# Kernel tuning notes

Measured on AMD Instinct MI355X. Metric: run time of the kernel, lower is better.

The kernel has to match this reference:

```python
import jax, jax.numpy as jnp
import numpy as np

K = 4
G = 64
IN_DIM = 256
OUT_DIM = 256
BATCH = 512
T0, T1 = -1.0, 1.0


def setup_inputs() -> dict:
    key = jax.random.key(0)
    kx, kw = jax.random.split(key)
    x = jax.random.uniform(kx, (BATCH, IN_DIM), jnp.float32, T0, T1)
    # xavier_normal_ on [G+K, in, out]: std = sqrt(2 / (fan_in + fan_out)) with fan over last two dims
    std = (2.0 / (IN_DIM + OUT_DIM)) ** 0.5
    w = jax.random.normal(kw, (G + K, IN_DIM, OUT_DIM), jnp.float32) * std
    # knot vector: k-1 repeats of t0, linspace(t0,t1,G+1), k-1 repeats of t1
    t = jnp.concatenate([
        jnp.full((K - 1,), T0, jnp.float32),
        jnp.linspace(T0, T1, G + 1, dtype=jnp.float32),
        jnp.full((K - 1,), T1, jnp.float32),
    ])
    return {"x": x, "w": w, "t": t, "k": K}


def _basis(x, t, k):
    """Cox-de Boor: the k nonzero order-k B-spline basis values at each x.
    Returns (idx, N): idx [..., k] basis indices i-k+1..i, N [..., k] values."""
    n_t = t.shape[0]
    # interval i with t[i] <= x < t[i+1], clipped to the valid span
    i = jnp.clip(jnp.searchsorted(t, x, side='right') - 1, k - 1, n_t - k - 1)
    N = jnp.ones(x.shape + (1,), x.dtype)
    for p in range(1, k):  # static small loop (k=4)
        jj = jnp.arange(1, p + 1)
        left = x[..., None] - t[i[..., None] + 1 - jj]   # [..., p]
        right = t[i[..., None] + jj] - x[..., None]      # [..., p]
        saved = jnp.zeros_like(x)
        vals = []
        for r in range(p):
            d = right[..., r] + left[..., p - 1 - r]      # t[i+r+1] - t[i+r+1-p]
            temp = N[..., r] / d
            vals.append(saved + right[..., r] * temp)
            saved = left[..., p - 1 - r] * temp
        vals.append(saved)
        N = jnp.stack(vals, -1)
    idx = i[..., None] - (k - 1) + jnp.arange(k)
    return idx, N


def reference(x, w, t, k):
    in_dim = x.shape[1]
    n_rows = w.shape[0]
    idx, y1 = _basis(x, t, k)                             # [B,in,k], [B,in,k]
    # last row of w (index -1 == n_rows-1) weights the SiLU residual term
    idx_full = jnp.concatenate(
        [idx, jnp.full(idx.shape[:-1] + (1,), n_rows - 1, idx.dtype)], -1)  # [B,in,k+1]
    silu = x * jax.nn.sigmoid(x)
    y2 = jnp.concatenate([y1, silu[..., None]], -1)       # [B,in,k+1]
    # gather local spline coefficients: w2[b,c,j,o] = w[idx_full[b,c,j], c, o]
    w2 = w[idx_full, jnp.arange(in_dim)[None, :, None], :]  # [B,in,k+1,out]
    return jnp.einsum('bcjo,bcj->bo', w2, y2)             # [B,out]
```

## Files before the change

### kernel.cpp

```cpp
#include <hip/hip_runtime.h>
#include <math.h>

#define IN_DIM  256
#define OUT_DIM 256
#define NROWS   68
#define NT      71
#define BATCH   512

__global__ __launch_bounds__(256) void kan_gather_kernel(
    const float* __restrict__ x, const float* __restrict__ w,
    const float* __restrict__ t, float* __restrict__ out) {
  __shared__ float  lt[NT];
  __shared__ float4 lyv[64];
  __shared__ float  lys[64];
  __shared__ int    lbase[64];
  __shared__ float4 red4[4][64];

  const int tid = threadIdx.x;
  const unsigned bid = blockIdx.x;
  const int sl = (bid & 7) >> 1;
  const int b  = ((bid & 1) << 8) | (bid >> 3);

  if (tid < NT) lt[tid] = t[tid];
  __syncthreads();

  if (tid < 64) {
    const int c = sl * 64 + tid;
    const float xv = x[b * IN_DIM + c];
    int i = 3 + (int)floorf((xv + 1.0f) * 32.0f);
    i = i < 3 ? 3 : (i > 66 ? 66 : i);
    while (i > 3 && xv < lt[i]) --i;
    while (i < 66 && xv >= lt[i + 1]) ++i;

    float N0 = 1.f, N1 = 0.f, N2 = 0.f, N3 = 0.f;
    {
      const float l1 = xv - lt[i];
      const float r1 = lt[i + 1] - xv;
      const float tp = N0 / (r1 + l1);
      N1 = l1 * tp;
      N0 = r1 * tp;
    }
    {
      const float l1 = xv - lt[i];
      const float l2 = xv - lt[i - 1];
      const float r1 = lt[i + 1] - xv;
      const float r2 = lt[i + 2] - xv;
      float saved = 0.f;
      const float tp0 = N0 / (r1 + l2);
      const float n0 = saved + r1 * tp0; saved = l2 * tp0;
      const float tp1 = N1 / (r2 + l1);
      const float n1 = saved + r2 * tp1; saved = l1 * tp1;
      N0 = n0; N1 = n1; N2 = saved;
    }
    {
      const float l1 = xv - lt[i];
      const float l2 = xv - lt[i - 1];
      const float l3 = xv - lt[i - 2];
      const float r1 = lt[i + 1] - xv;
      const float r2 = lt[i + 2] - xv;
      const float r3 = lt[i + 3] - xv;
      float saved = 0.f;
      const float tp0 = N0 / (r1 + l3);
      const float n0 = saved + r1 * tp0; saved = l3 * tp0;
      const float tp1 = N1 / (r2 + l2);
      const float n1 = saved + r2 * tp1; saved = l2 * tp1;
      const float tp2 = N2 / (r3 + l1);
      const float n2 = saved + r3 * tp2; saved = l1 * tp2;
      N0 = n0; N1 = n1; N2 = n2; N3 = saved;
    }
    lyv[tid]   = make_float4(N0, N1, N2, N3);
    lys[tid]   = xv / (1.0f + expf(-xv));
    lbase[tid] = i - 3;
  }
  __syncthreads();

  const int oq = tid & 63;
  const int cs = tid >> 6;
  const float4* __restrict__ w4 = (const float4*)w;

  float4 acc = make_float4(0.f, 0.f, 0.f, 0.f);
  const int cbeg = cs * 16;
  #pragma unroll 2
  for (int m = 0; m < 16; ++m) {
    const int cl = cbeg + m;
    const float4 yv = lyv[cl];
    const float  ys = lys[cl];
    const int base  = lbase[cl];
    const float4* p = w4 + (sl * 64 + cl) * 64 + oq;
    const float4 a0 = p[(base + 0) * 16384];
    const float4 a1 = p[(base + 1) * 16384];
    const float4 a2 = p[(base + 2) * 16384];
    const float4 a3 = p[(base + 3) * 16384];
    const float4 a4 = p[67 * 16384];
    acc.x += yv.x * a0.x + yv.y * a1.x + yv.z * a2.x + yv.w * a3.x + ys * a4.x;
    acc.y += yv.x * a0.y + yv.y * a1.y + yv.z * a2.y + yv.w * a3.y + ys * a4.y;
    acc.z += yv.x * a0.z + yv.y * a1.z + yv.z * a2.z + yv.w * a3.z + ys * a4.z;
    acc.w += yv.x * a0.w + yv.y * a1.w + yv.z * a2.w + yv.w * a3.w + ys * a4.w;
  }

  red4[cs][oq] = acc;
  __syncthreads();
  if (tid < 64) {
    const float4 p0 = red4[0][oq];
    const float4 p1 = red4[1][oq];
    const float4 p2 = red4[2][oq];
    const float4 p3 = red4[3][oq];
    float* op = out + b * OUT_DIM + oq * 4;
    atomicAdd(op + 0, (p0.x + p1.x) + (p2.x + p3.x));
    atomicAdd(op + 1, (p0.y + p1.y) + (p2.y + p3.y));
    atomicAdd(op + 2, (p0.z + p1.z) + (p2.z + p3.z));
    atomicAdd(op + 3, (p0.w + p1.w) + (p2.w + p3.w));
  }
}

extern "C" void kernel_launch(void* const* d_in, const int* in_sizes, int n_in,
                              void* d_out, int out_size, void* d_ws, size_t ws_size,
                              hipStream_t stream) {
  const float* x = (const float*)d_in[0];
  const float* w = (const float*)d_in[1];
  const float* t = (const float*)d_in[2];
  float* out = (float*)d_out;
  hipMemsetAsync(out, 0, (size_t)out_size * sizeof(float), stream);
  kan_gather_kernel<<<BATCH * 4, 256, 0, stream>>>(x, w, t, out);
}
```

Measured before the change: 95.41 us.

## Convert weights to bf16 in a pre-pass and gather half-width rows

Adds a conversion kernel that rounds the full fp32 weight tensor to bf16 in workspace on every call. The gather kernel then reads bf16 weights as uint4 (8 outputs per thread), so each gathered row carries half the bytes, and the cross-thread reduction is reorganised into 8 channel slices over 32 output lanes. The conversion pass itself reads all weights and writes half, which is about as much traffic as the gather saves. It also lowers the weight precision.

```diff
diff --git a/kernel.cpp b/kernel.cpp
--- a/kernel.cpp
+++ b/kernel.cpp
@@ -1,20 +1,51 @@
 #include <hip/hip_runtime.h>
 #include <math.h>
+#include <stdint.h>
 
 #define IN_DIM  256
 #define OUT_DIM 256
 #define NROWS   68
 #define NT      71
 #define BATCH   512
+#define W_ELEMS (NROWS * IN_DIM * OUT_DIM)
+
+__device__ __forceinline__ uint32_t bf16_rne(float f) {
+  uint32_t u = __builtin_bit_cast(uint32_t, f);
+  return (u + 0x7fffu + ((u >> 16) & 1u)) >> 16;
+}
+
+__global__ __launch_bounds__(256) void cvt_kernel(const float* __restrict__ w,
+                                                  uint32_t* __restrict__ wb) {
+  const int base = (blockIdx.x * 256 + threadIdx.x) * 8;
+  const float4 a = *(const float4*)(w + base);
+  const float4 b = *(const float4*)(w + base + 4);
+  uint4 o;
+  o.x = bf16_rne(a.x) | (bf16_rne(a.y) << 16);
+  o.y = bf16_rne(a.z) | (bf16_rne(a.w) << 16);
+  o.z = bf16_rne(b.x) | (bf16_rne(b.y) << 16);
+  o.w = bf16_rne(b.z) | (bf16_rne(b.w) << 16);
+  *(uint4*)(wb + base / 2) = o;
+}
+
+__device__ __forceinline__ void fma8(const uint4 q, const float y, float* acc) {
+  acc[0] += y * __builtin_bit_cast(float, q.x << 16);
+  acc[1] += y * __builtin_bit_cast(float, q.x & 0xffff0000u);
+  acc[2] += y * __builtin_bit_cast(float, q.y << 16);
+  acc[3] += y * __builtin_bit_cast(float, q.y & 0xffff0000u);
+  acc[4] += y * __builtin_bit_cast(float, q.z << 16);
+  acc[5] += y * __builtin_bit_cast(float, q.z & 0xffff0000u);
+  acc[6] += y * __builtin_bit_cast(float, q.w << 16);
+  acc[7] += y * __builtin_bit_cast(float, q.w & 0xffff0000u);
+}
 
 __global__ __launch_bounds__(256) void kan_gather_kernel(
-    const float* __restrict__ x, const float* __restrict__ w,
+    const float* __restrict__ x, const uint4* __restrict__ wp,
     const float* __restrict__ t, float* __restrict__ out) {
   __shared__ float  lt[NT];
   __shared__ float4 lyv[64];
   __shared__ float  lys[64];
   __shared__ int    lbase[64];
-  __shared__ float4 red4[4][64];
+  __shared__ float  red[8 * 32 * 9];
 
   const int tid = threadIdx.x;
   const unsigned bid = blockIdx.x;
@@ -37,8 +68,7 @@
       const float l1 = xv - lt[i];
       const float r1 = lt[i + 1] - xv;
       const float tp = N0 / (r1 + l1);
-      N1 = l1 * tp;
-      N0 = r1 * tp;
+      N1 = l1 * tp; N0 = r1 * tp;
     }
     {
       const float l1 = xv - lt[i];
@@ -74,42 +104,43 @@
   }
   __syncthreads();
 
-  const int oq = tid & 63;
-  const int cs = tid >> 6;
-  const float4* __restrict__ w4 = (const float4*)w;
+  const int ol = tid & 31;
+  const int cs = tid >> 5;
 
-  float4 acc = make_float4(0.f, 0.f, 0.f, 0.f);
-  const int cbeg = cs * 16;
+  float acc[8] = {0.f, 0.f, 0.f, 0.f, 0.f, 0.f, 0.f, 0.f};
+  const int cbeg = cs * 8;
   #pragma unroll 2
-  for (int m = 0; m < 16; ++m) {
+  for (int m = 0; m < 8; ++m) {
     const int cl = cbeg + m;
     const float4 yv = lyv[cl];
     const float  ys = lys[cl];
     const int base  = lbase[cl];
-    const float4* p = w4 + (sl * 64 + cl) * 64 + oq;
-    const float4 a0 = p[(base + 0) * 16384];
-    const float4 a1 = p[(base + 1) * 16384];
-    const float4 a2 = p[(base + 2) * 16384];
-    const float4 a3 = p[(base + 3) * 16384];
-    const float4 a4 = p[67 * 16384];
-    acc.x += yv.x * a0.x + yv.y * a1.x + yv.z * a2.x + yv.w * a3.x + ys * a4.x;
-    acc.y += yv.x * a0.y + yv.y * a1.y + yv.z * a2.y + yv.w * a3.y + ys * a4.y;
-    acc.z += yv.x * a0.z + yv.y * a1.z + yv.z * a2.z + yv.w * a3.z + ys * a4.z;
-    acc.w += yv.x * a0.w + yv.y * a1.w + yv.z * a2.w + yv.w * a3.w + ys * a4.w;
+    const uint4* p  = wp + (size_t)(sl * 64 + cl) * 32 + ol;
+    const uint4 q0 = p[(size_t)(base + 0) * 8192];
+    const uint4 q1 = p[(size_t)(base + 1) * 8192];
+    const uint4 q2 = p[(size_t)(base + 2) * 8192];
+    const uint4 q3 = p[(size_t)(base + 3) * 8192];
+    const uint4 q4 = p[(size_t)67 * 8192];
+    fma8(q0, yv.x, acc);
+    fma8(q1, yv.y, acc);
+    fma8(q2, yv.z, acc);
+    fma8(q3, yv.w, acc);
+    fma8(q4, ys,   acc);
   }
 
-  red4[cs][oq] = acc;
+  float* r = &red[(cs * 32 + ol) * 9];
+  #pragma unroll
+  for (int j = 0; j < 8; ++j) r[j] = acc[j];
   __syncthreads();
-  if (tid < 64) {
-    const float4 p0 = red4[0][oq];
-    const float4 p1 = red4[1][oq];
-    const float4 p2 = red4[2][oq];
-    const float4 p3 = red4[3][oq];
-    float* op = out + b * OUT_DIM + oq * 4;
-    atomicAdd(op + 0, (p0.x + p1.x) + (p2.x + p3.x));
-    atomicAdd(op + 1, (p0.y + p1.y) + (p2.y + p3.y));
-    atomicAdd(op + 2, (p0.z + p1.z) + (p2.z + p3.z));
-    atomicAdd(op + 3, (p0.w + p1.w) + (p2.w + p3.w));
+  if (tid < 32) {
+    float* op = out + b * OUT_DIM + ol * 8;
+    #pragma unroll
+    for (int j = 0; j < 8; ++j) {
+      float s = 0.f;
+      #pragma unroll
+      for (int sI = 0; sI < 8; ++sI) s += red[(sI * 32 + ol) * 9 + j];
+      atomicAdd(op + j, s);
+    }
   }
 }
 
@@ -120,6 +151,8 @@
   const float* w = (const float*)d_in[1];
   const float* t = (const float*)d_in[2];
   float* out = (float*)d_out;
+  uint32_t* wb = (uint32_t*)d_ws;
   hipMemsetAsync(out, 0, (size_t)out_size * sizeof(float), stream);
-  kan_gather_kernel<<<BATCH * 4, 256, 0, stream>>>(x, w, t, out);
+  cvt_kernel<<<W_ELEMS / (256 * 8), 256, 0, stream>>>(w, wb);
+  kan_gather_kernel<<<BATCH * 4, 256, 0, stream>>>(x, (const uint4*)wb, t, out);
 }
```

Measured after the change: 96.92 us. Within noise of the previous version (+1.6%).
